# Performance work log

Measured on AMD Instinct MI355X. Metric: run time of the kernel, lower is better.

The kernel has to match this reference:

```python
import jax, jax.numpy as jnp
import numpy as np

N, IN_DIM, INTER, HID, OUT, G = 8192, 512, 512, 1024, 512, 16
EPS = 1e-5


def setup_inputs() -> dict:
    key = jax.random.key(0)
    ks = jax.random.split(key, 16)
    s = 0.02
    return {
        "h": jax.random.normal(ks[0], (N, IN_DIM), jnp.float32),
        "D": jax.random.uniform(ks[1], (N, N), jnp.float32),
        "h_prime": jax.random.normal(ks[2], (N, OUT), jnp.float32),
        "Qw": jax.random.normal(ks[3], (IN_DIM, INTER), jnp.float32) * s,
        "Qb": jnp.zeros((INTER,), jnp.float32),
        "Kw": jax.random.normal(ks[4], (IN_DIM, INTER), jnp.float32) * s,
        "Kb": jnp.zeros((INTER,), jnp.float32),
        "Vw": jax.random.normal(ks[5], (IN_DIM, INTER), jnp.float32) * s,
        "Vb": jnp.zeros((INTER,), jnp.float32),
        "Rw": jax.random.normal(ks[6], (INTER, HID), jnp.float32) * s,
        "Rb": jnp.zeros((HID,), jnp.float32),
        "Cw": jax.random.normal(ks[7], (OUT, HID), jnp.float32) * s,
        "Cb": jnp.zeros((HID,), jnp.float32),
        "Pw": jax.random.normal(ks[8], (2 * HID, OUT), jnp.float32) * s,
        "Pb": jnp.zeros((OUT,), jnp.float32),
        "prelu_a": jnp.full((OUT,), 0.25, jnp.float32),  # PReLU default init
        "gn_w": jnp.ones((OUT,), jnp.float32),
        "gn_b": jnp.zeros((OUT,), jnp.float32),
    }


def reference(h, D, h_prime, Qw, Qb, Kw, Kb, Vw, Vb, Rw, Rb, Cw, Cb, Pw, Pb, prelu_a, gn_w, gn_b):
    Q = h @ Qw + Qb                      # (N, inter)
    K = h @ Kw + Kb
    V = h @ Vw + Vb
    scores = D * (Q @ K.T)               # (N, N), decayed retention scores
    h_ret = scores @ V                   # (N, inter)
    h_ret = jax.nn.gelu(h_ret @ Rw + Rb, approximate=False)   # (N, hid)
    h_cat = h_prime @ Cw + Cb            # (N, hid)
    combined = jnp.concatenate([h_ret, h_cat], axis=-1)       # (N, 2*hid)
    x = combined @ Pw + Pb               # (N, out)
    x = jnp.where(x >= 0, x, prelu_a * x)                      # PReLU per-channel
    # GroupNorm over channel groups per row: (N, G, out/G)
    xg = x.reshape(N, G, OUT // G)
    mu = xg.mean(axis=-1, keepdims=True)
    var = xg.var(axis=-1, keepdims=True)
    xn = ((xg - mu) * jax.lax.rsqrt(var + EPS)).reshape(N, OUT)
    return xn * gn_w + gn_b
```

## Files before the change

kernel.cpp:

```cpp
#include <hip/hip_runtime.h>
#include <math.h>

typedef __attribute__((ext_vector_type(8))) short bf16x8;
typedef __attribute__((ext_vector_type(4))) float f32x4;
typedef __attribute__((ext_vector_type(8))) unsigned short u16x8;

#define DEVFN __device__ __forceinline__
#define AS1 __attribute__((address_space(1)))
#define AS3 __attribute__((address_space(3)))

DEVFN unsigned short f2bf(float f) {
    unsigned int u = __float_as_uint(f);
    u += 0x7fffu + ((u >> 16) & 1u);
    return (unsigned short)(u >> 16);
}

__global__ void cast2_kernel(const float* __restrict__ a, const float* __restrict__ b,
                             unsigned short* __restrict__ oa, unsigned short* __restrict__ ob,
                             int n8) {
    const float* in = blockIdx.y ? b : a;
    unsigned short* out = blockIdx.y ? ob : oa;
    int i = blockIdx.x * blockDim.x + threadIdx.x;
    if (i >= n8) return;
    const float4* p = reinterpret_cast<const float4*>(in) + (size_t)i * 2;
    float4 x = p[0], y = p[1];
    u16x8 o;
    o[0] = f2bf(x.x); o[1] = f2bf(x.y); o[2] = f2bf(x.z); o[3] = f2bf(x.w);
    o[4] = f2bf(y.x); o[5] = f2bf(y.y); o[6] = f2bf(y.z); o[7] = f2bf(y.w);
    reinterpret_cast<u16x8*>(out)[i] = o;
}

__global__ void sum4_cast_kernel(const float* __restrict__ p, size_t stride,
                                 unsigned short* __restrict__ out, int n8) {
    int i = blockIdx.x * blockDim.x + threadIdx.x;
    if (i >= n8) return;
    const float4* a = reinterpret_cast<const float4*>(p) + (size_t)i * 2;
    const float4* b = reinterpret_cast<const float4*>(p + stride) + (size_t)i * 2;
    const float4* c = reinterpret_cast<const float4*>(p + 2 * stride) + (size_t)i * 2;
    const float4* d = reinterpret_cast<const float4*>(p + 3 * stride) + (size_t)i * 2;
    u16x8 o;
#pragma unroll
    for (int j = 0; j < 2; ++j) {
        float4 va = a[j], vb = b[j], vc = c[j], vd = d[j];
        o[4 * j + 0] = f2bf(va.x + vb.x + vc.x + vd.x);
        o[4 * j + 1] = f2bf(va.y + vb.y + vc.y + vd.y);
        o[4 * j + 2] = f2bf(va.z + vb.z + vc.z + vd.z);
        o[4 * j + 3] = f2bf(va.w + vb.w + vc.w + vd.w);
    }
    reinterpret_cast<u16x8*>(out)[i] = o;
}

__global__ void concat_bias_kernel(const float* __restrict__ a,
                                   const float* __restrict__ b,
                                   const float* __restrict__ c,
                                   float* __restrict__ o) {
    int i = blockIdx.x * blockDim.x + threadIdx.x;
    if (i >= 1536) return;
    o[i] = i < 512 ? a[i] : (i < 1024 ? b[i - 512] : c[i - 1024]);
}

struct TD { const float* in; unsigned short* out; int ldin, ldout, nbx, nby; };
struct TD6 { TD d[6]; };

__global__ void multi_transpose_kernel(TD6 t6) {
    TD d = t6.d[blockIdx.z];
    if ((int)blockIdx.x >= d.nbx || (int)blockIdx.y >= d.nby) return;
    __shared__ unsigned short tile[32][34];
    int c0 = blockIdx.x * 32, r0 = blockIdx.y * 32;
    int tx = threadIdx.x, ty = threadIdx.y;
#pragma unroll
    for (int i = 0; i < 32; i += 8)
        tile[ty + i][tx] = f2bf(d.in[(size_t)(r0 + ty + i) * d.ldin + c0 + tx]);
    __syncthreads();
#pragma unroll
    for (int i = 0; i < 32; i += 8)
        d.out[(size_t)(c0 + ty + i) * d.ldout + r0 + tx] = tile[tx][ty + i];
}

__global__ void transpose_bf16_kernel(const unsigned short* __restrict__ in, int ldin,
                                      unsigned short* __restrict__ out, int ldout) {
    __shared__ unsigned short tile[32][34];
    int c0 = blockIdx.x * 32, r0 = blockIdx.y * 32;
    int tx = threadIdx.x, ty = threadIdx.y;
#pragma unroll
    for (int i = 0; i < 32; i += 8)
        tile[ty + i][tx] = in[(size_t)(r0 + ty + i) * ldin + c0 + tx];
    __syncthreads();
#pragma unroll
    for (int i = 0; i < 32; i += 8)
        out[(size_t)(c0 + ty + i) * ldout + r0 + tx] = tile[tx][ty + i];
}

enum { P8_DMUL = 0, P8_F32 = 1 };

#define DSR(dst, base, IMM) \
    asm volatile("ds_read_b128 %0, %1 offset:%c2" : "=v"(dst) : "v"(base), "i"(IMM))

#define DSA(MHOFF)                                \
    DSR(areg[0][0], abase0, (MHOFF) + 0 * 4096);  \
    DSR(areg[0][1], abase1, (MHOFF) + 0 * 4096);  \
    DSR(areg[1][0], abase0, (MHOFF) + 1 * 4096);  \
    DSR(areg[1][1], abase1, (MHOFF) + 1 * 4096);  \
    DSR(areg[2][0], abase0, (MHOFF) + 2 * 4096);  \
    DSR(areg[2][1], abase1, (MHOFF) + 2 * 4096);  \
    DSR(areg[3][0], abase0, (MHOFF) + 3 * 4096);  \
    DSR(areg[3][1], abase1, (MHOFF) + 3 * 4096);

#define DSB(BR, NHOFF)                            \
    DSR(BR[0][0], bbase0, (NHOFF) + 0 * 8192);    \
    DSR(BR[0][1], bbase1, (NHOFF) + 0 * 8192);    \
    DSR(BR[1][0], bbase0, (NHOFF) + 1 * 8192);    \
    DSR(BR[1][1], bbase1, (NHOFF) + 1 * 8192);

#define STAGEA(BUF, HALF, KT)                                                   \
    {                                                                           \
        const unsigned short* g0 = Ablk + (size_t)((HALF) * 128 + srow) * lda + (KT) * 64 + src8;       \
        const unsigned short* g1 = Ablk + (size_t)((HALF) * 128 + 64 + srow) * lda + (KT) * 64 + src8;  \
        unsigned short* d0 = &As[BUF][(HALF) * 8192 + (w * 64) * 8];            \
        unsigned short* d1 = &As[BUF][(HALF) * 8192 + (512 + w * 64) * 8];      \
        __builtin_amdgcn_global_load_lds((const AS1 void*)g0, (AS3 void*)d0, 16, 0, 0); \
        __builtin_amdgcn_global_load_lds((const AS1 void*)g1, (AS3 void*)d1, 16, 0, 0); \
    }

#define STAGEB(BUF, HALF, KT)                                                   \
    {                                                                           \
        const unsigned short* g0 = Bblk + (size_t)((HALF) * 128 + srow) * ldb + (KT) * 64 + src8;       \
        const unsigned short* g1 = Bblk + (size_t)((HALF) * 128 + 64 + srow) * ldb + (KT) * 64 + src8;  \
        unsigned short* d0 = &Bs[BUF][(HALF) * 8192 + (w * 64) * 8];            \
        unsigned short* d1 = &Bs[BUF][(HALF) * 8192 + (512 + w * 64) * 8];      \
        __builtin_amdgcn_global_load_lds((const AS1 void*)g0, (AS3 void*)d0, 16, 0, 0); \
        __builtin_amdgcn_global_load_lds((const AS1 void*)g1, (AS3 void*)d1, 16, 0, 0); \
    }

#define MMAC(BR, MB, NB)                                                        \
    {                                                                           \
        __builtin_amdgcn_s_setprio(1);                                          \
        _Pragma("unroll") for (int q = 0; q < 4; ++q)                           \
        _Pragma("unroll") for (int p = 0; p < 2; ++p)                           \
        _Pragma("unroll") for (int kk = 0; kk < 2; ++kk)                        \
            acc[(MB) + q][(NB) + p] = __builtin_amdgcn_mfma_f32_16x16x32_bf16(  \
                areg[q][kk], BR[p][kk], acc[(MB) + q][(NB) + p], 0, 0, 0);      \
        __builtin_amdgcn_s_setprio(0);                                          \
    }

#define VMCNT6 asm volatile("s_waitcnt vmcnt(6)" ::: "memory")
#define VMCNT0 asm volatile("s_waitcnt vmcnt(0)" ::: "memory")
#define BAR __builtin_amdgcn_s_barrier()
#define WAITDS                                          \
    asm volatile("s_waitcnt lgkmcnt(0)" ::: "memory");  \
    __builtin_amdgcn_sched_barrier(0)

template <int MODE>
__global__ __launch_bounds__(512, 2) void gemm8p_kernel(
    const unsigned short* __restrict__ A, int lda,
    const unsigned short* __restrict__ B, int ldb,
    void* __restrict__ Cv, int ldc, int K,
    const float* __restrict__ Dmul, int ldd, size_t zstride) {
    __shared__ alignas(16) unsigned short As[2][256 * 64];
    __shared__ alignas(16) unsigned short Bs[2][256 * 64];

    unsigned bx, by, zi = 0;
    if (MODE == P8_F32) {
        unsigned gx = gridDim.x;
        unsigned L = (blockIdx.z * gridDim.y + blockIdx.y) * gx + blockIdx.x;
        unsigned xcd = L & 7u, slot = L >> 3;
        zi = xcd >> 1;
        unsigned t = slot * 2 + (xcd & 1u);
        bx = t & (gx - 1);
        by = t / gx;
    } else {
        unsigned nwg = gridDim.x * gridDim.y;
        unsigned bid = blockIdx.y * gridDim.x + blockIdx.x;
        unsigned cpx = nwg >> 3;
        bid = (bid & 7u) * cpx + (bid >> 3);
        bx = bid % gridDim.x;
        by = bid / gridDim.x;
    }
    size_t m0 = (size_t)by * 256, n0 = (size_t)bx * 256;

    int tid = threadIdx.x;
    int lane = tid & 63, w = tid >> 6;
    int wm = w >> 2, wn = w & 3;
    int lrow = lane & 15;

    const unsigned short* Ablk = A + m0 * lda + (size_t)zi * K;
    const unsigned short* Bblk = B + n0 * ldb + (size_t)zi * K;
    int src8 = ((lane & 7) ^ (lane >> 3)) * 8;
    int srow = w * 8 + (lane >> 3);

    unsigned asBase = (unsigned)(uintptr_t)(AS3 const void*)&As[0][0];
    unsigned bsBase = (unsigned)(uintptr_t)(AS3 const void*)&Bs[0][0];
    unsigned cA0 = (unsigned)((((lane >> 4)) ^ (lane & 7)) * 16);
    unsigned cA1 = (unsigned)(((4 + (lane >> 4)) ^ (lane & 7)) * 16);
    unsigned aOff0 = asBase + (unsigned)((wm * 16 + lrow) * 128);
    unsigned bOff0 = bsBase + (unsigned)((wn * 16 + lrow) * 128);

    f32x4 acc[8][4];
#pragma unroll
    for (int i = 0; i < 8; ++i)
#pragma unroll
        for (int j = 0; j < 4; ++j)
#pragma unroll
            for (int r = 0; r < 4; ++r) acc[i][j][r] = 0.f;

    const int NT = K >> 6;

    STAGEA(0, 0, 0); STAGEB(0, 0, 0); STAGEB(0, 1, 0); STAGEA(0, 1, 0);
    if (NT > 1) { STAGEA(1, 0, 1); STAGEB(1, 0, 1); STAGEB(1, 1, 1); }
    if (NT > 1) { VMCNT6; } else { VMCNT0; }
    BAR;

    bf16x8 areg[4][2], breg0[2][2], breg1[2][2];

    for (int t = 0; t < NT; ++t) {
        int buf = t & 1;
        unsigned boff = (unsigned)buf * 32768u;
        unsigned abase0 = aOff0 + boff + cA0;
        unsigned abase1 = aOff0 + boff + cA1;
        unsigned bbase0 = bOff0 + boff + cA0;
        unsigned bbase1 = bOff0 + boff + cA1;

        DSA(0);
        DSB(breg0, 0);
        if (t + 1 < NT) STAGEA(buf ^ 1, 1, t + 1);
        BAR;
        WAITDS;
        MMAC(breg0, 0, 0);
        BAR;
        DSB(breg1, 16384);
        if (t + 2 < NT) STAGEA(buf, 0, t + 2);
        BAR;
        WAITDS;
        MMAC(breg1, 0, 2);
        BAR;
        DSA(16384);
        if (t + 2 < NT) STAGEB(buf, 0, t + 2);
        BAR;
        WAITDS;
        MMAC(breg1, 4, 2);
        BAR;
        if (t + 2 < NT) { STAGEB(buf, 1, t + 2); VMCNT6; } else { VMCNT0; }
        BAR;
        MMAC(breg0, 4, 0);
        BAR;
    }

#pragma unroll
    for (int mi = 0; mi < 8; ++mi) {
#pragma unroll
        for (int ni = 0; ni < 4; ++ni) {
            size_t gcol = n0 + ni * 64 + wn * 16 + (lane & 15);
#pragma unroll
            for (int r = 0; r < 4; ++r) {
                size_t grow = m0 + mi * 32 + wm * 16 + ((lane >> 4) << 2) + r;
                if (MODE == P8_DMUL) {
                    float v = acc[mi][ni][r] * Dmul[grow * (size_t)ldd + gcol];
                    ((unsigned short*)Cv)[grow * (size_t)ldc + gcol] = f2bf(v);
                } else {
                    float* Cf = (float*)Cv + zi * zstride;
                    Cf[grow * (size_t)ldc + gcol] = acc[mi][ni][r];
                }
            }
        }
    }
}

enum { EP_BF16_BIAS = 0, EP_PRELU_GN = 4, EP_DUAL = 5 };

template <int MODE>
__global__ __launch_bounds__(256, 2) void gemm_bt_kernel(
    const unsigned short* __restrict__ A, int lda,
    const unsigned short* __restrict__ B, int ldb,
    void* __restrict__ Cv, int ldc, int K,
    const float* __restrict__ bias,
    const float* __restrict__ PA, const float* __restrict__ GW,
    const float* __restrict__ GB,
    const unsigned short* __restrict__ A2,
    const unsigned short* __restrict__ B2,
    const float* __restrict__ bias2) {
    __shared__ alignas(16) unsigned short As[2][128 * 64];
    __shared__ alignas(16) unsigned short Bs[2][128 * 64];

    unsigned nwg = gridDim.x * gridDim.y;
    unsigned bid = blockIdx.y * gridDim.x + blockIdx.x;
    unsigned cpx = nwg >> 3;
    bid = (bid & 7u) * cpx + (bid >> 3);
    unsigned bx = bid % gridDim.x, by = bid / gridDim.x;
    size_t m0 = (size_t)by * 128;
    size_t nB = (size_t)bx * 128;
    size_t ncol0 = nB;

    const unsigned short* Ause = A;
    const unsigned short* Buse = B;
    const float* bias_use = bias;
    bool apply_gelu = false;
    if (MODE == EP_DUAL) {
        unsigned half = gridDim.x >> 1;
        if (bx >= half) {
            nB = (size_t)(bx - half) * 128;
            ncol0 = 1024 + nB;
            Ause = A2; Buse = B2; bias_use = bias2;
        } else {
            apply_gelu = true;
        }
    }

    int tid = threadIdx.x;
    int lane = tid & 63, w = tid >> 6;
    int wr = w >> 1, wc = w & 1;
    int cif = lane & 15;
    int rif = (lane >> 4) << 2;

    f32x4 acc[4][4];
#pragma unroll
    for (int i = 0; i < 4; ++i)
#pragma unroll
        for (int j = 0; j < 4; ++j)
#pragma unroll
            for (int r = 0; r < 4; ++r) acc[i][j][r] = 0.f;

    const unsigned short* Ablk = Ause + m0 * lda;
    const unsigned short* Bblk = Buse + nB * ldb;
    int srccol = ((lane & 7) ^ (lane >> 3)) * 8;
    int srow = w * 32 + (lane >> 3);
    int nkt = K >> 6;

    auto stage = [&](int buf, int kt) {
        int k0 = kt << 6;
        unsigned short* la = &As[buf][w * 2048];
        unsigned short* lb = &Bs[buf][w * 2048];
#pragma unroll
        for (int i = 0; i < 4; ++i) {
            __builtin_amdgcn_global_load_lds(
                (const AS1 void*)(Ablk + (size_t)(srow + i * 8) * lda + k0 + srccol),
                (AS3 void*)(la + i * 512), 16, 0, 0);
            __builtin_amdgcn_global_load_lds(
                (const AS1 void*)(Bblk + (size_t)(srow + i * 8) * ldb + k0 + srccol),
                (AS3 void*)(lb + i * 512), 16, 0, 0);
        }
    };

    stage(0, 0);
    __syncthreads();

    for (int kt = 0; kt < nkt; ++kt) {
        int cur = kt & 1;
        if (kt + 1 < nkt) stage(cur ^ 1, kt + 1);

        const bf16x8* Ap = reinterpret_cast<const bf16x8*>(As[cur]);
        const bf16x8* Bp = reinterpret_cast<const bf16x8*>(Bs[cur]);
#pragma unroll
        for (int kk = 0; kk < 2; ++kk) {
            bf16x8 af[4], bfr[4];
#pragma unroll
            for (int mi = 0; mi < 4; ++mi) {
                int row = wr * 64 + mi * 16 + (lane & 15);
                int slot = ((kk << 2) + (lane >> 4)) ^ (row & 7);
                af[mi] = Ap[row * 8 + slot];
            }
#pragma unroll
            for (int ni = 0; ni < 4; ++ni) {
                int row = wc * 64 + ni * 16 + (lane & 15);
                int slot = ((kk << 2) + (lane >> 4)) ^ (row & 7);
                bfr[ni] = Bp[row * 8 + slot];
            }
#pragma unroll
            for (int mi = 0; mi < 4; ++mi)
#pragma unroll
                for (int ni = 0; ni < 4; ++ni)
                    acc[mi][ni] = __builtin_amdgcn_mfma_f32_16x16x32_bf16(
                        af[mi], bfr[ni], acc[mi][ni], 0, 0, 0);
        }
        __syncthreads();
    }

    if (MODE == EP_PRELU_GN) {
        float* Cf = (float*)Cv;
        float pbv[4], pav[4], gwv[4], gbv[4];
        size_t gcolv[4];
#pragma unroll
        for (int ni = 0; ni < 4; ++ni) {
            gcolv[ni] = ncol0 + wc * 64 + ni * 16 + cif;
            pbv[ni] = bias[gcolv[ni]];
            pav[ni] = PA[gcolv[ni]];
            gwv[ni] = GW[gcolv[ni]];
            gbv[ni] = GB[gcolv[ni]];
        }
#pragma unroll
        for (int mi = 0; mi < 4; ++mi) {
#pragma unroll
            for (int ni = 0; ni < 4; ++ni)
#pragma unroll
                for (int r = 0; r < 4; ++r) {
                    float v = acc[mi][ni][r] + pbv[ni];
                    acc[mi][ni][r] = v >= 0.f ? v : pav[ni] * v;
                }
#pragma unroll
            for (int p = 0; p < 2; ++p) {
                float s[4], ss[4];
#pragma unroll
                for (int r = 0; r < 4; ++r) {
                    float a0 = acc[mi][2 * p][r], a1 = acc[mi][2 * p + 1][r];
                    s[r] = a0 + a1;
                    ss[r] = a0 * a0 + a1 * a1;
                }
#pragma unroll
                for (int msk = 1; msk < 16; msk <<= 1)
#pragma unroll
                    for (int r = 0; r < 4; ++r) {
                        s[r] += __shfl_xor(s[r], msk);
                        ss[r] += __shfl_xor(ss[r], msk);
                    }
#pragma unroll
                for (int r = 0; r < 4; ++r) {
                    float mu = s[r] * (1.f / 32.f);
                    float inv = rsqrtf(ss[r] * (1.f / 32.f) - mu * mu + 1e-5f);
                    size_t grow = m0 + wr * 64 + mi * 16 + rif + r;
#pragma unroll
                    for (int q = 0; q < 2; ++q) {
                        int ni = 2 * p + q;
                        Cf[grow * (size_t)ldc + gcolv[ni]] =
                            (acc[mi][ni][r] - mu) * inv * gwv[ni] + gbv[ni];
                    }
                }
            }
        }
        return;
    }

#pragma unroll
    for (int mi = 0; mi < 4; ++mi) {
#pragma unroll
        for (int ni = 0; ni < 4; ++ni) {
            size_t gcol = ncol0 + wc * 64 + ni * 16 + cif;
            size_t bcol = nB + wc * 64 + ni * 16 + cif;
            float bval = bias_use ? bias_use[bcol] : 0.f;
#pragma unroll
            for (int r = 0; r < 4; ++r) {
                size_t grow = m0 + wr * 64 + mi * 16 + rif + r;
                float val = acc[mi][ni][r] + bval;
                if (MODE == EP_DUAL && apply_gelu)
                    val = 0.5f * val * (1.f + erff(val * 0.70710678118654752f));
                ((unsigned short*)Cv)[grow * (size_t)ldc + gcol] = f2bf(val);
            }
        }
    }
}

extern "C" void kernel_launch(void* const* d_in, const int* in_sizes, int n_in,
                              void* d_out, int out_size, void* d_ws, size_t ws_size,
                              hipStream_t stream) {
    constexpr int Nn = 8192, IND = 512, INTER = 512, HID = 1024, OUTD = 512;
    const float* h   = (const float*)d_in[0];
    const float* Dm  = (const float*)d_in[1];
    const float* hp  = (const float*)d_in[2];
    const float* Qw  = (const float*)d_in[3];
    const float* Qb  = (const float*)d_in[4];
    const float* Kw  = (const float*)d_in[5];
    const float* Kb  = (const float*)d_in[6];
    const float* Vw  = (const float*)d_in[7];
    const float* Vb  = (const float*)d_in[8];
    const float* Rw  = (const float*)d_in[9];
    const float* Rb  = (const float*)d_in[10];
    const float* Cw  = (const float*)d_in[11];
    const float* Cb  = (const float*)d_in[12];
    const float* Pw  = (const float*)d_in[13];
    const float* Pb  = (const float*)d_in[14];
    const float* pa  = (const float*)d_in[15];
    const float* gwt = (const float*)d_in[16];
    const float* gbt = (const float*)d_in[17];
    (void)in_sizes; (void)n_in; (void)out_size; (void)ws_size;

    char* ws = (char*)d_ws;
    size_t cur = 0;
    auto alloc = [&](size_t bytes) -> void* {
        void* p = ws + cur;
        cur += (bytes + 255) & ~(size_t)255;
        return p;
    };
    unsigned short* h_bf   = (unsigned short*)alloc((size_t)Nn * IND * 2);
    unsigned short* hp_bf  = (unsigned short*)alloc((size_t)Nn * OUTD * 2);
    unsigned short* QKVwT  = (unsigned short*)alloc((size_t)3 * INTER * IND * 2);
    float*          qkvb   = (float*)alloc((size_t)3 * INTER * 4);
    unsigned short* RwT    = (unsigned short*)alloc((size_t)INTER * HID * 2);
    unsigned short* CwT    = (unsigned short*)alloc((size_t)OUTD * HID * 2);
    unsigned short* PwT    = (unsigned short*)alloc((size_t)2 * HID * OUTD * 2);
    unsigned short* QKVm   = (unsigned short*)alloc((size_t)Nn * 3 * INTER * 2);
    unsigned short* VTm    = (unsigned short*)alloc((size_t)Nn * INTER * 2);
    unsigned short* Sm     = (unsigned short*)alloc((size_t)Nn * Nn * 2);
    float*          hret32 = (float*)alloc((size_t)4 * Nn * INTER * 4);
    unsigned short* hretbf = (unsigned short*)alloc((size_t)Nn * INTER * 2);
    unsigned short* comb   = Sm;

    unsigned short* Qm = QKVm;
    unsigned short* Km = QKVm + INTER;
    unsigned short* Vm = QKVm + 2 * INTER;
    const int ldqkv = 3 * INTER;

    dim3 tb(32, 8);
    int n8 = Nn * IND / 8;
    cast2_kernel<<<dim3(n8 / 256, 2), 256, 0, stream>>>(h, hp, h_bf, hp_bf, n8);

    TD6 t6;
    t6.d[0] = {Qw, QKVwT,                          INTER, IND,     16, 16};
    t6.d[1] = {Kw, QKVwT + (size_t)INTER * IND,    INTER, IND,     16, 16};
    t6.d[2] = {Vw, QKVwT + (size_t)2 * INTER * IND,INTER, IND,     16, 16};
    t6.d[3] = {Rw, RwT,                            HID,   INTER,   32, 16};
    t6.d[4] = {Cw, CwT,                            HID,   OUTD,    32, 16};
    t6.d[5] = {Pw, PwT,                            OUTD,  2 * HID, 16, 64};
    multi_transpose_kernel<<<dim3(32, 64, 6), tb, 0, stream>>>(t6);
    concat_bias_kernel<<<6, 256, 0, stream>>>(Qb, Kb, Vb, qkvb);

    gemm_bt_kernel<EP_BF16_BIAS><<<dim3(3 * INTER / 128, Nn / 128), 256, 0, stream>>>(
        h_bf, IND, QKVwT, IND, QKVm, ldqkv, IND, qkvb,
        nullptr, nullptr, nullptr, nullptr, nullptr, nullptr);
    transpose_bf16_kernel<<<dim3(INTER / 32, Nn / 32), tb, 0, stream>>>(Vm, ldqkv, VTm, Nn);

    gemm8p_kernel<P8_DMUL><<<dim3(Nn / 256, Nn / 256), 512, 0, stream>>>(
        Qm, ldqkv, Km, ldqkv, Sm, Nn, INTER, Dm, Nn, 0);

    gemm8p_kernel<P8_F32><<<dim3(OUTD / 256, Nn / 256, 4), 512, 0, stream>>>(
        Sm, Nn, VTm, Nn, hret32, INTER, Nn / 4, nullptr, 0, (size_t)Nn * INTER);
    sum4_cast_kernel<<<(Nn * INTER / 8) / 256, 256, 0, stream>>>(
        hret32, (size_t)Nn * INTER, hretbf, Nn * INTER / 8);

    gemm_bt_kernel<EP_DUAL><<<dim3(2 * HID / 128, Nn / 128), 256, 0, stream>>>(
        hretbf, INTER, RwT, INTER, comb, 2 * HID, INTER, Rb,
        nullptr, nullptr, nullptr, hp_bf, CwT, Cb);

    gemm_bt_kernel<EP_PRELU_GN><<<dim3(OUTD / 128, Nn / 128), 256, 0, stream>>>(
        comb, 2 * HID, PwT, 2 * HID, d_out, OUTD, 2 * HID, Pb,
        pa, gwt, gbt, nullptr, nullptr, nullptr);
}
```

Measured before the change: 378.1 us.

## Replace 8-phase GEMM pipeline with simple double-buffered loop and prefetched D

After: 637.8 us. +68.7%, slower.

```diff
diff --git a/kernel.cpp b/kernel.cpp
--- a/kernel.cpp
+++ b/kernel.cpp
@@ -96,21 +96,13 @@
 #define DSR(dst, base, IMM) \
     asm volatile("ds_read_b128 %0, %1 offset:%c2" : "=v"(dst) : "v"(base), "i"(IMM))
 
-#define DSA(MHOFF)                                \
-    DSR(areg[0][0], abase0, (MHOFF) + 0 * 4096);  \
-    DSR(areg[0][1], abase1, (MHOFF) + 0 * 4096);  \
-    DSR(areg[1][0], abase0, (MHOFF) + 1 * 4096);  \
-    DSR(areg[1][1], abase1, (MHOFF) + 1 * 4096);  \
-    DSR(areg[2][0], abase0, (MHOFF) + 2 * 4096);  \
-    DSR(areg[2][1], abase1, (MHOFF) + 2 * 4096);  \
-    DSR(areg[3][0], abase0, (MHOFF) + 3 * 4096);  \
-    DSR(areg[3][1], abase1, (MHOFF) + 3 * 4096);
-
-#define DSB(BR, NHOFF)                            \
-    DSR(BR[0][0], bbase0, (NHOFF) + 0 * 8192);    \
-    DSR(BR[0][1], bbase1, (NHOFF) + 0 * 8192);    \
-    DSR(BR[1][0], bbase0, (NHOFF) + 1 * 8192);    \
-    DSR(BR[1][1], bbase1, (NHOFF) + 1 * 8192);
+#define DSA2(mi)                                  \
+    DSR(areg[mi][0], abase0, (mi) * 4096);        \
+    DSR(areg[mi][1], abase1, (mi) * 4096);
+
+#define DSB2(ni)                                  \
+    DSR(breg[ni][0], bbase0, (ni) * 8192);        \
+    DSR(breg[ni][1], bbase1, (ni) * 8192);
 
 #define STAGEA(BUF, HALF, KT)                                                   \
     {                                                                           \
@@ -132,18 +124,24 @@
         __builtin_amdgcn_global_load_lds((const AS1 void*)g1, (AS3 void*)d1, 16, 0, 0); \
     }
 
-#define MMAC(BR, MB, NB)                                                        \
+#define STAGE_ALL(BUF, KT) \
+    STAGEA(BUF, 0, KT); STAGEB(BUF, 0, KT); STAGEB(BUF, 1, KT); STAGEA(BUF, 1, KT)
+
+#define DS_ALL                                                      \
+    DSA2(0) DSA2(1) DSA2(2) DSA2(3) DSA2(4) DSA2(5) DSA2(6) DSA2(7) \
+    DSB2(0) DSB2(1) DSB2(2) DSB2(3)
+
+#define MMAC_ALL                                                                \
     {                                                                           \
         __builtin_amdgcn_s_setprio(1);                                          \
-        _Pragma("unroll") for (int q = 0; q < 4; ++q)                           \
-        _Pragma("unroll") for (int p = 0; p < 2; ++p)                           \
+        _Pragma("unroll") for (int mi = 0; mi < 8; ++mi)                        \
+        _Pragma("unroll") for (int ni = 0; ni < 4; ++ni)                        \
         _Pragma("unroll") for (int kk = 0; kk < 2; ++kk)                        \
-            acc[(MB) + q][(NB) + p] = __builtin_amdgcn_mfma_f32_16x16x32_bf16(  \
-                areg[q][kk], BR[p][kk], acc[(MB) + q][(NB) + p], 0, 0, 0);      \
+            acc[mi][ni] = __builtin_amdgcn_mfma_f32_16x16x32_bf16(              \
+                areg[mi][kk], breg[ni][kk], acc[mi][ni], 0, 0, 0);              \
         __builtin_amdgcn_s_setprio(0);                                          \
     }
 
-#define VMCNT6 asm volatile("s_waitcnt vmcnt(6)" ::: "memory")
 #define VMCNT0 asm volatile("s_waitcnt vmcnt(0)" ::: "memory")
 #define BAR __builtin_amdgcn_s_barrier()
 #define WAITDS                                          \
@@ -151,7 +149,7 @@
     __builtin_amdgcn_sched_barrier(0)
 
 template <int MODE>
-__global__ __launch_bounds__(512, 2) void gemm8p_kernel(
+__global__ __launch_bounds__(512, 2) void gemm2p_kernel(
     const unsigned short* __restrict__ A, int lda,
     const unsigned short* __restrict__ B, int ldb,
     void* __restrict__ Cv, int ldc, int K,
@@ -204,15 +202,14 @@
             for (int r = 0; r < 4; ++r) acc[i][j][r] = 0.f;
 
     const int NT = K >> 6;
-
-    STAGEA(0, 0, 0); STAGEB(0, 0, 0); STAGEB(0, 1, 0); STAGEA(0, 1, 0);
-    if (NT > 1) { STAGEA(1, 0, 1); STAGEB(1, 0, 1); STAGEB(1, 1, 1); }
-    if (NT > 1) { VMCNT6; } else { VMCNT0; }
+    bf16x8 areg[8][2], breg[4][2];
+    float dreg[8][4][4];
+
+    STAGE_ALL(0, 0);
+    VMCNT0;
     BAR;
 
-    bf16x8 areg[4][2], breg0[2][2], breg1[2][2];
-
-    for (int t = 0; t < NT; ++t) {
+    for (int t = 0; t < NT - 1; ++t) {
         int buf = t & 1;
         unsigned boff = (unsigned)buf * 32768u;
         unsigned abase0 = aOff0 + boff + cA0;
@@ -220,29 +217,36 @@
         unsigned bbase0 = bOff0 + boff + cA0;
         unsigned bbase1 = bOff0 + boff + cA1;
 
-        DSA(0);
-        DSB(breg0, 0);
-        if (t + 1 < NT) STAGEA(buf ^ 1, 1, t + 1);
+        STAGE_ALL(buf ^ 1, t + 1);
+        DS_ALL;
+        WAITDS;
+        MMAC_ALL;
+        VMCNT0;
         BAR;
+    }
+
+    {
+        int buf = (NT - 1) & 1;
+        unsigned boff = (unsigned)buf * 32768u;
+        unsigned abase0 = aOff0 + boff + cA0;
+        unsigned abase1 = aOff0 + boff + cA1;
+        unsigned bbase0 = bOff0 + boff + cA0;
+        unsigned bbase1 = bOff0 + boff + cA1;
+
+        if (MODE == P8_DMUL) {
+#pragma unroll
+            for (int mi = 0; mi < 8; ++mi)
+#pragma unroll
+                for (int ni = 0; ni < 4; ++ni)
+#pragma unroll
+                    for (int r = 0; r < 4; ++r)
+                        dreg[mi][ni][r] =
+                            Dmul[(m0 + mi * 32 + wm * 16 + ((lane >> 4) << 2) + r) * (size_t)ldd +
+                                 (n0 + ni * 64 + wn * 16 + (lane & 15))];
+        }
+        DS_ALL;
         WAITDS;
-        MMAC(breg0, 0, 0);
-        BAR;
-        DSB(breg1, 16384);
-        if (t + 2 < NT) STAGEA(buf, 0, t + 2);
-        BAR;
-        WAITDS;
-        MMAC(breg1, 0, 2);
-        BAR;
-        DSA(16384);
-        if (t + 2 < NT) STAGEB(buf, 0, t + 2);
-        BAR;
-        WAITDS;
-        MMAC(breg1, 4, 2);
-        BAR;
-        if (t + 2 < NT) { STAGEB(buf, 1, t + 2); VMCNT6; } else { VMCNT0; }
-        BAR;
-        MMAC(breg0, 4, 0);
-        BAR;
+        MMAC_ALL;
     }
 
 #pragma unroll
@@ -254,7 +258,7 @@
             for (int r = 0; r < 4; ++r) {
                 size_t grow = m0 + mi * 32 + wm * 16 + ((lane >> 4) << 2) + r;
                 if (MODE == P8_DMUL) {
-                    float v = acc[mi][ni][r] * Dmul[grow * (size_t)ldd + gcol];
+                    float v = acc[mi][ni][r] * dreg[mi][ni][r];
                     ((unsigned short*)Cv)[grow * (size_t)ldc + gcol] = f2bf(v);
                 } else {
                     float* Cf = (float*)Cv + zi * zstride;
@@ -516,10 +520,10 @@
         nullptr, nullptr, nullptr, nullptr, nullptr, nullptr);
     transpose_bf16_kernel<<<dim3(INTER / 32, Nn / 32), tb, 0, stream>>>(Vm, ldqkv, VTm, Nn);
 
-    gemm8p_kernel<P8_DMUL><<<dim3(Nn / 256, Nn / 256), 512, 0, stream>>>(
+    gemm2p_kernel<P8_DMUL><<<dim3(Nn / 256, Nn / 256), 512, 0, stream>>>(
         Qm, ldqkv, Km, ldqkv, Sm, Nn, INTER, Dm, Nn, 0);
 
-    gemm8p_kernel<P8_F32><<<dim3(OUTD / 256, Nn / 256, 4), 512, 0, stream>>>(
+    gemm2p_kernel<P8_F32><<<dim3(OUTD / 256, Nn / 256, 4), 512, 0, stream>>>(
         Sm, Nn, VTm, Nn, hret32, INTER, Nn / 4, nullptr, 0, (size_t)Nn * INTER);
     sum4_cast_kernel<<<(Nn * INTER / 8) / 256, 256, 0, stream>>>(
         hret32, (size_t)Nn * INTER, hretbf, Nn * INTER / 8);
```
